# Optimization experiments

Hardware: AMD Instinct MI355X
Metric: run time of the kernel (lower is better)

## Reference

```python
import jax, jax.numpy as jnp
import numpy as np

V, BLOCK, E, H = 50257, 2048, 256, 8
DH = E // H  # head_size = 32
B, T = 2, 2048
SCALE = 1.0 / np.float32(np.sqrt(DH))


def setup_inputs() -> dict:
    key = jax.random.key(0)
    ks = jax.random.split(key, 9)
    s = 0.02
    return {
        "idx": jax.random.randint(ks[0], (B, T), 0, V),
        "targets": jax.random.randint(ks[1], (B, T), 0, V),
        "tok_emb": jax.random.normal(ks[2], (V, E), jnp.float32) * s,
        "pos_emb": jax.random.normal(ks[3], (BLOCK, E), jnp.float32) * s,
        "Wq": jax.random.normal(ks[4], (H, E, DH), jnp.float32) * s,
        "Wk": jax.random.normal(ks[5], (H, E, DH), jnp.float32) * s,
        "Wv": jax.random.normal(ks[6], (H, E, DH), jnp.float32) * s,
        "Wlm": jax.random.normal(ks[7], (V, E), jnp.float32) * s,
        "blm": jnp.zeros((V,), jnp.float32),
    }


def reference(idx, targets, tok_emb, pos_emb, Wq, Wk, Wv, Wlm, blm):
    t = idx.shape[1]
    x = tok_emb[idx] + pos_emb[:t]  # [B,T,E]
    # all heads batched (original loops over heads; same math)
    q = jnp.einsum('bte,hed->bhtd', x, Wq)
    k = jnp.einsum('bte,hed->bhtd', x, Wk)
    v = jnp.einsum('bte,hed->bhtd', x, Wv)
    scores = jnp.einsum('bhqd,bhkd->bhqk', q, k) * SCALE  # [B,H,T,T]
    causal = jnp.tril(jnp.ones((t, t), dtype=bool))
    # faithful to original: tril then masked_fill(scores == 0, -inf)
    scores = jnp.where(causal, scores, 0.0)
    scores = jnp.where(scores == 0.0, -jnp.inf, scores)
    # faithful to original bug: softmax over the QUERY axis (torch dim=1 of [b,t,t])
    attn = jax.nn.softmax(scores, axis=2)
    out = jnp.einsum('bhqk,bhkd->bqhd', attn, v).reshape(idx.shape[0], t, E)  # concat heads
    logits = out @ Wlm.T + blm  # [B,T,V]
    logp = jax.nn.log_softmax(logits, axis=-1)
    loss = -jnp.take_along_axis(logp, targets[..., None], axis=-1).mean()
    return logits, loss
```

## Files before the change

kernel.cpp:

```cpp
#include <hip/hip_runtime.h>
#include <hip/hip_bf16.h>
#include <cstdint>
#include <cstddef>

typedef __bf16 bf16x8 __attribute__((ext_vector_type(8)));
typedef __bf16 bf16x4 __attribute__((ext_vector_type(4)));
typedef float  f32x4  __attribute__((ext_vector_type(4)));
typedef float  f32x16 __attribute__((ext_vector_type(16)));

#define SCALE_QK 0.17677669529663687f
#define V_SIZE 50257
#define T_SEQ  2048
#define E_DIM  256
#define NROWS  4096
#define NNB    393
#define NPAD   (NNB * 128)

__device__ __forceinline__ f32x4 mfma16(bf16x8 a, bf16x8 b, f32x4 c) {
    return __builtin_amdgcn_mfma_f32_16x16x32_bf16(a, b, c, 0, 0, 0);
}
__device__ __forceinline__ f32x16 mfma32(bf16x8 a, bf16x8 b, f32x16 c) {
    return __builtin_amdgcn_mfma_f32_32x32x16_bf16(a, b, c, 0, 0, 0);
}

#define GLOAD_LDS16(gptr, lptr) \
    __builtin_amdgcn_global_load_lds((const __attribute__((address_space(1))) void*)(gptr), \
                                     (__attribute__((address_space(3))) void*)(lptr), 16, 0, 0)

#define ASM_VMCNT0 asm volatile("s_waitcnt vmcnt(0)" ::: "memory")

#define PREP_EMBED 1024
#define PREP_WQKV  (PREP_EMBED + 768)
#define PREP_CVT   (PREP_WQKV + 12576)
#define PREP_ZERO  (PREP_CVT + 128)
__global__ void __launch_bounds__(256)
k_prep(const int* __restrict__ idx, const float* __restrict__ tok,
       const float* __restrict__ pos, __bf16* __restrict__ X,
       const float* __restrict__ Wq, const float* __restrict__ Wk,
       const float* __restrict__ Wv, __bf16* __restrict__ Wo,
       const float* __restrict__ Wlm, __bf16* __restrict__ WlmB,
       float* __restrict__ Dcol) {
    const int bx = blockIdx.x, tid = threadIdx.x;
    if (bx < PREP_EMBED) {
        int row = bx * 4 + (tid >> 6);
        int tl = row & (T_SEQ - 1);
        int tk = idx[row];
        int e = (tid & 63) * 4;
        f32x4 a = *(const f32x4*)(tok + (size_t)tk * E_DIM + e);
        f32x4 p = *(const f32x4*)(pos + (size_t)tl * E_DIM + e);
        bf16x4 o;
#pragma unroll
        for (int i = 0; i < 4; ++i) o[i] = (__bf16)(a[i] + p[i]);
        *(bf16x4*)(X + (size_t)row * E_DIM + e) = o;
    } else if (bx < PREP_WQKV) {
        int n = bx - PREP_EMBED;
        int sel = n >> 8, hd = n & 255, h = hd >> 5, d = hd & 31;
        const float* W = (sel == 0) ? Wq : (sel == 1) ? Wk : Wv;
        Wo[(size_t)n * E_DIM + tid] = (__bf16)W[((size_t)h * E_DIM + tid) * 32 + d];
    } else if (bx < PREP_CVT) {
        size_t i = ((size_t)(bx - PREP_WQKV) * 256 + tid) * 4;
        bf16x4 o = {};
        if (i + 4 <= (size_t)V_SIZE * E_DIM) {
            f32x4 v = *(const f32x4*)(Wlm + i);
#pragma unroll
            for (int j = 0; j < 4; ++j) o[j] = (__bf16)v[j];
        }
        *(bf16x4*)(WlmB + i) = o;
    } else {
        Dcol[(bx - PREP_CVT) * 256 + tid] = 0.f;
    }
}

template <bool BF16_OUT, bool DO_EPI, int REP>
__global__ void __launch_bounds__(256)
k_gemm_bt(const __bf16* __restrict__ A, const __bf16* __restrict__ B,
          void* __restrict__ Cout, const float* __restrict__ bias,
          float* __restrict__ partials, int M, int N, int K) {
    __shared__ __align__(16) char smem[65536];
    __shared__ __align__(16) float bias_lds[128];
    __shared__ float wsum[128][2];

    const int tid = threadIdx.x;
    const int lane = tid & 63, w = tid >> 6;
    const int wr = w >> 1, wc = w & 1;
    const int bm = blockIdx.x, bn = blockIdx.y;
    const int brow = bm * 128, bcol = bn * 128;
    const int gg = lane >> 4, li = lane & 15;
    const int nt = K >> 6;

    if (DO_EPI && tid < 128) bias_lds[tid] = (bcol + tid < N) ? bias[bcol + tid] : 0.f;

    auto stage = [&](int t, int buf) {
        char* Ab = smem + buf * 32768;
        char* Bb = Ab + 16384;
#pragma unroll
        for (int i = 0; i < 4; ++i) {
            int cb = (w * 4 + i) * 64;
            int c = cb + lane;
            int r = c >> 3, kbs = (c & 7) ^ (r & 7);
            GLOAD_LDS16(A + (size_t)(brow + r) * K + t * 64 + kbs * 8, Ab + cb * 16);
            GLOAD_LDS16(B + (size_t)(bcol + r) * K + t * 64 + kbs * 8, Bb + cb * 16);
        }
    };

    for (int rep = 0; rep < REP; ++rep) {
        f32x4 acc[4][4] = {};

        stage(0, 0);
        ASM_VMCNT0;
        __builtin_amdgcn_s_barrier();
        __builtin_amdgcn_sched_barrier(0);

        int cur = 0;
        for (int t = 0; t < nt; ++t) {
            if (t + 1 < nt) stage(t + 1, cur ^ 1);
            const int cbase = cur * 32768;
#pragma unroll
            for (int ks = 0; ks < 2; ++ks) {
                bf16x8 af[4], bfr[4];
#pragma unroll
                for (int mi = 0; mi < 4; ++mi) {
                    int r = wr * 64 + mi * 16 + li;
                    int kbyte = (ks * 64 + gg * 16) ^ ((r & 7) << 4);
                    af[mi] = *(const bf16x8*)(smem + cbase + r * 128 + kbyte);
                }
#pragma unroll
                for (int ni = 0; ni < 4; ++ni) {
                    int r = wc * 64 + ni * 16 + li;
                    int kbyte = (ks * 64 + gg * 16) ^ ((r & 7) << 4);
                    bfr[ni] = *(const bf16x8*)(smem + cbase + 16384 + r * 128 + kbyte);
                }
#pragma unroll
                for (int mi = 0; mi < 4; ++mi)
#pragma unroll
                    for (int ni = 0; ni < 4; ++ni)
                        acc[mi][ni] = mfma16(bfr[ni], af[mi], acc[mi][ni]);
            }
            ASM_VMCNT0;
            __builtin_amdgcn_s_barrier();
            __builtin_amdgcn_sched_barrier(0);
            cur ^= 1;
        }

        const bool full = (bcol + 128 <= N);
        if constexpr (!DO_EPI) {
#pragma unroll
            for (int mi = 0; mi < 4; ++mi) {
                const size_t mrow = (size_t)(brow + wr * 64 + mi * 16 + li) * N;
#pragma unroll
                for (int ni = 0; ni < 4; ++ni) {
                    int nc = wc * 64 + ni * 16 + gg * 4;
                    f32x4 v = acc[mi][ni];
                    bf16x4 o;
#pragma unroll
                    for (int j = 0; j < 4; ++j) o[j] = (__bf16)v[j];
                    *(bf16x4*)((__bf16*)Cout + mrow + bcol + nc) = o;
                }
            }
        } else if (full) {
#pragma unroll
            for (int mi = 0; mi < 4; ++mi) {
                int row = wr * 64 + mi * 16 + li;
                float s = 0.f;
#pragma unroll
                for (int ni = 0; ni < 4; ++ni) {
                    int colb = (wc * 64 + ni * 16 + gg * 4) * 4;
                    f32x4 v = acc[mi][ni];
                    f32x4 bv = *(const f32x4*)((const char*)bias_lds + colb);
#pragma unroll
                    for (int j = 0; j < 4; ++j) { v[j] += bv[j]; s += __expf(v[j]); }
                    *(f32x4*)(smem + row * 512 + (colb ^ ((row & 7) << 4))) = v;
                }
                s += __shfl_xor(s, 16); s += __shfl_xor(s, 32);
                if (gg == 0) wsum[row][wc] = s;
            }
            __syncthreads();
#pragma unroll
            for (int i = 0; i < 16; ++i) {
                int o = i * 4096 + tid * 16;
                int row = o >> 9, cb = o & 511;
                f32x4 v = *(const f32x4*)(smem + row * 512 + (cb ^ ((row & 7) << 4)));
                *(f32x4*)((float*)Cout + (size_t)(brow + row) * N + bcol + (cb >> 2)) = v;
            }
        } else {
#pragma unroll
            for (int mi = 0; mi < 4; ++mi) {
                const size_t mrow = (size_t)(brow + wr * 64 + mi * 16 + li) * N;
                float s = 0.f;
#pragma unroll
                for (int ni = 0; ni < 4; ++ni) {
                    int nc = wc * 64 + ni * 16 + gg * 4;
#pragma unroll
                    for (int j = 0; j < 4; ++j) {
                        int col = bcol + nc + j;
                        if (col < N) {
                            float v = acc[mi][ni][j] + bias_lds[nc + j];
                            s += __expf(v);
                            ((float*)Cout)[mrow + col] = v;
                        }
                    }
                }
                s += __shfl_xor(s, 16); s += __shfl_xor(s, 32);
                if (gg == 0) wsum[wr * 64 + mi * 16 + li][wc] = s;
            }
        }
        if constexpr (DO_EPI) {
            __syncthreads();
            if (tid < 128)
                partials[(size_t)bn * NROWS + (brow + tid)] = wsum[tid][0] + wsum[tid][1];
        }
        if constexpr (REP > 1) __syncthreads();
    }
}

__global__ void __launch_bounds__(256)
k_pass1(const __bf16* __restrict__ QKV, float* __restrict__ Dcol) {
    int p = blockIdx.x;
    int kt = 0;
    while (p >= 16 - kt) { p -= 16 - kt; ++kt; }
    const int qc = kt + p;
    const int bh = blockIdx.y;
    const int b = bh >> 3, h = bh & 7;
    const int tid = threadIdx.x, lane = tid & 63, w = tid >> 6;
    const int g = lane >> 5, li = lane & 31;
    __shared__ __align__(16) __bf16 Klds[4 * 128 * 8];
    __shared__ __align__(16) __bf16 Qlds[4 * 128 * 8];

    const size_t baseQ = ((size_t)b * T_SEQ) * 768 + h * 32;
    const size_t baseK = baseQ + 256;

#pragma unroll
    for (int i = 0; i < 2; ++i) {
        int c = i * 256 + tid; int k = c >> 2, db = c & 3;
        *(bf16x8*)(Klds + (db * 128 + k) * 8) =
            *(const bf16x8*)(QKV + baseK + (size_t)(kt * 128 + k) * 768 + db * 8);
        *(bf16x8*)(Qlds + (db * 128 + k) * 8) =
            *(const bf16x8*)(QKV + baseQ + (size_t)(qc * 128 + k) * 768 + db * 8);
    }
    __syncthreads();

    float csum = 0.f;
    const int kglob = kt * 128 + w * 32 + li;
#pragma unroll
    for (int qs = 0; qs < 4; ++qs) {
        f32x16 sacc = {};
#pragma unroll
        for (int ks = 0; ks < 2; ++ks) {
            bf16x8 aq = *(const bf16x8*)(Qlds + ((ks * 2 + g) * 128 + qs * 32 + li) * 8);
            bf16x8 bk = *(const bf16x8*)(Klds + ((ks * 2 + g) * 128 + w * 32 + li) * 8);
            sacc = mfma32(aq, bk, sacc);
        }
#pragma unroll
        for (int r = 0; r < 16; ++r) {
            int qrow = qc * 128 + qs * 32 + ((r & 3) + 8 * (r >> 2) + 4 * g);
            if (kglob <= qrow) csum += __expf(sacc[r] * SCALE_QK);
        }
    }
    csum += __shfl_xor(csum, 32);
    if (g == 0) atomicAdd(&Dcol[(size_t)bh * T_SEQ + kglob], csum);
}

__global__ void __launch_bounds__(256)
k_pass2(const __bf16* __restrict__ QKV, const float* __restrict__ Dcol,
        float* __restrict__ Yf0, float* __restrict__ Yf1) {
    const int p = blockIdx.x, bh = blockIdx.y;
    const int pi = p >> 1, par = p & 1;
    const int b = bh >> 3, h = bh & 7;
    const int tid = threadIdx.x, lane = tid & 63, w = tid >> 6;
    const int g = lane >> 5, li = lane & 31;
    float* __restrict__ Yf = par ? Yf1 : Yf0;
    __shared__ __align__(16) __bf16 Qlds[4 * 128 * 8];
    __shared__ __align__(16) __bf16 Klds[4 * 128 * 8];
    __shared__ __align__(16) __bf16 UT[16 * 32 * 8];
    __shared__ __align__(16) __bf16 Plds[4][32 * 136];

    const size_t baseQ = ((size_t)b * T_SEQ) * 768 + h * 32;
    const size_t baseK = baseQ + 256;
    const size_t baseV = baseQ + 512;

#pragma unroll
    for (int ti = 0; ti < 2; ++ti) {
        const int qt = ti ? (15 - pi) : pi;
        __syncthreads();
#pragma unroll
        for (int i = 0; i < 2; ++i) {
            int c = i * 256 + tid; int q = c >> 2, db = c & 3;
            *(bf16x8*)(Qlds + (db * 128 + q) * 8) =
                *(const bf16x8*)(QKV + baseQ + (size_t)(qt * 128 + q) * 768 + db * 8);
        }
        f32x16 oacc = {};
        const int qrow = qt * 128 + w * 32 + li;

        for (int kc = par; kc <= qt; kc += 2) {
            __syncthreads();
#pragma unroll
            for (int i = 0; i < 2; ++i) {
                int c = i * 256 + tid; int k = c >> 2, db = c & 3;
                *(bf16x8*)(Klds + (db * 128 + k) * 8) =
                    *(const bf16x8*)(QKV + baseK + (size_t)(kc * 128 + k) * 768 + db * 8);
            }
#pragma unroll
            for (int i = 0; i < 4; ++i) {
                int c = i * 256 + tid; int k = c & 127, d4 = c >> 7;
                float rD = 1.0f / Dcol[(size_t)bh * T_SEQ + kc * 128 + k];
                bf16x4 v4 = *(const bf16x4*)(QKV + baseV + (size_t)(kc * 128 + k) * 768 + d4 * 4);
                int kb = k >> 3, j = k & 7;
#pragma unroll
                for (int t2 = 0; t2 < 4; ++t2)
                    UT[((size_t)kb * 32 + d4 * 4 + t2) * 8 + j] = (__bf16)((float)v4[t2] * rD);
            }
            __syncthreads();

#pragma unroll
            for (int ksub = 0; ksub < 4; ++ksub) {
                int kbase = kc * 128 + ksub * 32;
                f32x16 sacc = {};
#pragma unroll
                for (int ks = 0; ks < 2; ++ks) {
                    bf16x8 ak = *(const bf16x8*)(Klds + ((ks * 2 + g) * 128 + ksub * 32 + li) * 8);
                    bf16x8 bq = *(const bf16x8*)(Qlds + ((ks * 2 + g) * 128 + w * 32 + li) * 8);
                    sacc = mfma32(ak, bq, sacc);
                }
                float pv[16];
#pragma unroll
                for (int r = 0; r < 16; ++r) {
                    int kk = kbase + (r & 3) + 8 * (r >> 2) + 4 * g;
                    pv[r] = (kk <= qrow) ? __expf(sacc[r] * SCALE_QK) : 0.f;
                }
#pragma unroll
                for (int t2 = 0; t2 < 4; ++t2) {
                    bf16x4 pk;
#pragma unroll
                    for (int e = 0; e < 4; ++e) pk[e] = (__bf16)pv[4 * t2 + e];
                    *(bf16x4*)(&Plds[w][li * 136 + ksub * 32 + 8 * t2 + 4 * g]) = pk;
                }
            }
#pragma unroll
            for (int ks16 = 0; ks16 < 8; ++ks16) {
                bf16x8 ap = *(const bf16x8*)(&Plds[w][li * 136 + ks16 * 16 + g * 8]);
                bf16x8 bu = *(const bf16x8*)(UT + ((ks16 * 2 + g) * 32 + li) * 8);
                oacc = mfma32(ap, bu, oacc);
            }
        }
#pragma unroll
        for (int r = 0; r < 16; ++r) {
            int q = qt * 128 + w * 32 + (r & 3) + 8 * (r >> 2) + 4 * g;
            Yf[((size_t)b * T_SEQ + q) * E_DIM + h * 32 + li] = oacc[r];
        }
    }
}

__global__ void k_ycvt(const float* __restrict__ a, const float* __restrict__ b,
                       __bf16* __restrict__ y, int n4) {
    int i = blockIdx.x * 256 + threadIdx.x;
    if (i < n4) {
        f32x4 va = ((const f32x4*)a)[i], vb = ((const f32x4*)b)[i];
        bf16x4 o;
#pragma unroll
        for (int j = 0; j < 4; ++j) o[j] = (__bf16)(va[j] + vb[j]);
        ((bf16x4*)y)[i] = o;
    }
}

__global__ void k_rowlse(const float* __restrict__ partials, const float* __restrict__ logits,
                         const int* __restrict__ tgt, float* __restrict__ rowloss) {
    int r = blockIdx.x * 256 + threadIdx.x;
    float s = 0.f;
    for (int i = 0; i < NNB; ++i) s += partials[(size_t)i * NROWS + r];
    float lse = logf(s);
    rowloss[r] = lse - logits[(size_t)r * V_SIZE + tgt[r]];
}

__global__ void k_loss(const float* __restrict__ rowloss, float* __restrict__ out) {
    __shared__ float red[4];
    float s = 0.f;
    for (int i = threadIdx.x; i < NROWS; i += 256) s += rowloss[i];
    for (int m = 1; m < 64; m <<= 1) s += __shfl_xor(s, m);
    if ((threadIdx.x & 63) == 0) red[threadIdx.x >> 6] = s;
    __syncthreads();
    if (threadIdx.x == 0) out[0] = (red[0] + red[1] + red[2] + red[3]) / (float)NROWS;
}

extern "C" void kernel_launch(void* const* d_in, const int* in_sizes, int n_in,
                              void* d_out, int out_size, void* d_ws, size_t ws_size,
                              hipStream_t stream) {
    const int*   idx = (const int*)d_in[0];
    const int*   tgt = (const int*)d_in[1];
    const float* tok = (const float*)d_in[2];
    const float* pos = (const float*)d_in[3];
    const float* Wq  = (const float*)d_in[4];
    const float* Wk  = (const float*)d_in[5];
    const float* Wv  = (const float*)d_in[6];
    const float* Wlm = (const float*)d_in[7];
    const float* blm = (const float*)d_in[8];

    float* logits = (float*)d_out;
    float* loss   = logits + (size_t)NROWS * V_SIZE;

    char* ws = (char*)d_ws;
    __bf16* X        = (__bf16*)ws; ws += (size_t)NROWS * E_DIM * 2;
    __bf16* Wqkv     = (__bf16*)ws; ws += (size_t)768 * E_DIM * 2;
    __bf16* QKV      = (__bf16*)ws; ws += (size_t)NROWS * 768 * 2;
    float*  Dcol     = (float*)ws;  ws += (size_t)16 * T_SEQ * 4;
    __bf16* Y        = (__bf16*)ws; ws += (size_t)NROWS * E_DIM * 2;
    float*  Yf0      = (float*)ws;  ws += (size_t)NROWS * E_DIM * 4;
    float*  Yf1      = (float*)ws;  ws += (size_t)NROWS * E_DIM * 4;
    __bf16* WlmB     = (__bf16*)ws; ws += (size_t)NPAD * E_DIM * 2;
    float*  partials = (float*)ws;  ws += (size_t)NNB * NROWS * 4;
    float*  rowloss  = (float*)ws;  ws += (size_t)NROWS * 4;

    k_prep<<<PREP_ZERO, 256, 0, stream>>>(idx, tok, pos, X, Wq, Wk, Wv, Wqkv,
                                          Wlm, WlmB, Dcol);
    k_gemm_bt<true, false, 1><<<dim3(NROWS / 128, 768 / 128), 256, 0, stream>>>(
        X, Wqkv, QKV, nullptr, nullptr, NROWS, 768, E_DIM);
    k_pass1<<<dim3(136, 16), 256, 0, stream>>>(QKV, Dcol);
    k_pass2<<<dim3(16, 16), 256, 0, stream>>>(QKV, Dcol, Yf0, Yf1);
    k_ycvt<<<(NROWS * E_DIM / 4 + 255) / 256, 256, 0, stream>>>(Yf0, Yf1, Y, NROWS * E_DIM / 4);
    k_gemm_bt<false, true, 1><<<dim3(NROWS / 128, NNB), 256, 0, stream>>>(
        Y, WlmB, logits, blm, partials, NROWS, V_SIZE, E_DIM);
    k_rowlse<<<NROWS / 256, 256, 0, stream>>>(partials, logits, tgt, rowloss);
    k_loss<<<1, 256, 0, stream>>>(rowloss, loss);
}
```

Before: 482.5 us.

## Single-buffer GEMM with compile-time K, higher occupancy and direct epilogue stores

```diff
diff --git a/kernel.cpp b/kernel.cpp
--- a/kernel.cpp
+++ b/kernel.cpp
@@ -26,8 +26,6 @@
 #define GLOAD_LDS16(gptr, lptr) \
     __builtin_amdgcn_global_load_lds((const __attribute__((address_space(1))) void*)(gptr), \
                                      (__attribute__((address_space(3))) void*)(lptr), 16, 0, 0)
-
-#define ASM_VMCNT0 asm volatile("s_waitcnt vmcnt(0)" ::: "memory")
 
 #define PREP_EMBED 1024
 #define PREP_WQKV  (PREP_EMBED + 768)
@@ -71,12 +69,13 @@
     }
 }
 
-template <bool BF16_OUT, bool DO_EPI, int REP>
-__global__ void __launch_bounds__(256)
+template <bool BF16_OUT, bool DO_EPI, int KK>
+__global__ void __launch_bounds__(256, 4)
 k_gemm_bt(const __bf16* __restrict__ A, const __bf16* __restrict__ B,
           void* __restrict__ Cout, const float* __restrict__ bias,
-          float* __restrict__ partials, int M, int N, int K) {
-    __shared__ __align__(16) char smem[65536];
+          float* __restrict__ partials, int M, int N) {
+    __shared__ __align__(16) __bf16 Alds[128 * 64];
+    __shared__ __align__(16) __bf16 Blds[128 * 64];
     __shared__ __align__(16) float bias_lds[128];
     __shared__ float wsum[128][2];
 
@@ -86,130 +85,104 @@
     const int bm = blockIdx.x, bn = blockIdx.y;
     const int brow = bm * 128, bcol = bn * 128;
     const int gg = lane >> 4, li = lane & 15;
-    const int nt = K >> 6;
+
+    f32x4 acc[4][4] = {};
 
     if (DO_EPI && tid < 128) bias_lds[tid] = (bcol + tid < N) ? bias[bcol + tid] : 0.f;
 
-    auto stage = [&](int t, int buf) {
-        char* Ab = smem + buf * 32768;
-        char* Bb = Ab + 16384;
+#pragma unroll
+    for (int t = 0; t < KK / 64; ++t) {
 #pragma unroll
         for (int i = 0; i < 4; ++i) {
             int cb = (w * 4 + i) * 64;
             int c = cb + lane;
             int r = c >> 3, kbs = (c & 7) ^ (r & 7);
-            GLOAD_LDS16(A + (size_t)(brow + r) * K + t * 64 + kbs * 8, Ab + cb * 16);
-            GLOAD_LDS16(B + (size_t)(bcol + r) * K + t * 64 + kbs * 8, Bb + cb * 16);
-        }
-    };
-
-    for (int rep = 0; rep < REP; ++rep) {
-        f32x4 acc[4][4] = {};
-
-        stage(0, 0);
-        ASM_VMCNT0;
-        __builtin_amdgcn_s_barrier();
-        __builtin_amdgcn_sched_barrier(0);
-
-        int cur = 0;
-        for (int t = 0; t < nt; ++t) {
-            if (t + 1 < nt) stage(t + 1, cur ^ 1);
-            const int cbase = cur * 32768;
-#pragma unroll
-            for (int ks = 0; ks < 2; ++ks) {
-                bf16x8 af[4], bfr[4];
-#pragma unroll
-                for (int mi = 0; mi < 4; ++mi) {
-                    int r = wr * 64 + mi * 16 + li;
-                    int kbyte = (ks * 64 + gg * 16) ^ ((r & 7) << 4);
-                    af[mi] = *(const bf16x8*)(smem + cbase + r * 128 + kbyte);
-                }
-#pragma unroll
-                for (int ni = 0; ni < 4; ++ni) {
-                    int r = wc * 64 + ni * 16 + li;
-                    int kbyte = (ks * 64 + gg * 16) ^ ((r & 7) << 4);
-                    bfr[ni] = *(const bf16x8*)(smem + cbase + 16384 + r * 128 + kbyte);
-                }
-#pragma unroll
-                for (int mi = 0; mi < 4; ++mi)
-#pragma unroll
-                    for (int ni = 0; ni < 4; ++ni)
-                        acc[mi][ni] = mfma16(bfr[ni], af[mi], acc[mi][ni]);
-            }
-            ASM_VMCNT0;
-            __builtin_amdgcn_s_barrier();
-            __builtin_amdgcn_sched_barrier(0);
-            cur ^= 1;
-        }
-
-        const bool full = (bcol + 128 <= N);
-        if constexpr (!DO_EPI) {
+            GLOAD_LDS16(A + (size_t)(brow + r) * KK + t * 64 + kbs * 8, (char*)Alds + cb * 16);
+            GLOAD_LDS16(B + (size_t)(bcol + r) * KK + t * 64 + kbs * 8, (char*)Blds + cb * 16);
+        }
+        __syncthreads();
+#pragma unroll
+        for (int ks = 0; ks < 2; ++ks) {
+            bf16x8 af[4], bfr[4];
 #pragma unroll
             for (int mi = 0; mi < 4; ++mi) {
-                const size_t mrow = (size_t)(brow + wr * 64 + mi * 16 + li) * N;
-#pragma unroll
-                for (int ni = 0; ni < 4; ++ni) {
-                    int nc = wc * 64 + ni * 16 + gg * 4;
-                    f32x4 v = acc[mi][ni];
+                int r = wr * 64 + mi * 16 + li;
+                int kbyte = (ks * 64 + gg * 16) ^ ((r & 7) << 4);
+                af[mi] = *(const bf16x8*)((const char*)Alds + r * 128 + kbyte);
+            }
+#pragma unroll
+            for (int ni = 0; ni < 4; ++ni) {
+                int r = wc * 64 + ni * 16 + li;
+                int kbyte = (ks * 64 + gg * 16) ^ ((r & 7) << 4);
+                bfr[ni] = *(const bf16x8*)((const char*)Blds + r * 128 + kbyte);
+            }
+#pragma unroll
+            for (int mi = 0; mi < 4; ++mi)
+#pragma unroll
+                for (int ni = 0; ni < 4; ++ni)
+                    acc[mi][ni] = mfma16(bfr[ni], af[mi], acc[mi][ni]);
+        }
+        if (t + 1 < KK / 64) __syncthreads();
+    }
+
+    const bool full = (bcol + 128 <= N);
+    if (full) {
+#pragma unroll
+        for (int mi = 0; mi < 4; ++mi) {
+            const size_t mrow = (size_t)(brow + wr * 64 + mi * 16 + li) * N;
+            float s = 0.f;
+#pragma unroll
+            for (int ni = 0; ni < 4; ++ni) {
+                int nc = wc * 64 + ni * 16 + gg * 4;
+                f32x4 v = acc[mi][ni];
+                if constexpr (DO_EPI) {
+                    f32x4 bv = *(const f32x4*)&bias_lds[nc];
+#pragma unroll
+                    for (int j = 0; j < 4; ++j) { v[j] += bv[j]; s += __expf(v[j]); }
+                }
+                if constexpr (BF16_OUT) {
                     bf16x4 o;
 #pragma unroll
                     for (int j = 0; j < 4; ++j) o[j] = (__bf16)v[j];
                     *(bf16x4*)((__bf16*)Cout + mrow + bcol + nc) = o;
-                }
-            }
-        } else if (full) {
-#pragma unroll
-            for (int mi = 0; mi < 4; ++mi) {
-                int row = wr * 64 + mi * 16 + li;
-                float s = 0.f;
-#pragma unroll
-                for (int ni = 0; ni < 4; ++ni) {
-                    int colb = (wc * 64 + ni * 16 + gg * 4) * 4;
-                    f32x4 v = acc[mi][ni];
-                    f32x4 bv = *(const f32x4*)((const char*)bias_lds + colb);
-#pragma unroll
-                    for (int j = 0; j < 4; ++j) { v[j] += bv[j]; s += __expf(v[j]); }
-                    *(f32x4*)(smem + row * 512 + (colb ^ ((row & 7) << 4))) = v;
-                }
-                s += __shfl_xor(s, 16); s += __shfl_xor(s, 32);
-                if (gg == 0) wsum[row][wc] = s;
-            }
-            __syncthreads();
-#pragma unroll
-            for (int i = 0; i < 16; ++i) {
-                int o = i * 4096 + tid * 16;
-                int row = o >> 9, cb = o & 511;
-                f32x4 v = *(const f32x4*)(smem + row * 512 + (cb ^ ((row & 7) << 4)));
-                *(f32x4*)((float*)Cout + (size_t)(brow + row) * N + bcol + (cb >> 2)) = v;
-            }
-        } else {
-#pragma unroll
-            for (int mi = 0; mi < 4; ++mi) {
-                const size_t mrow = (size_t)(brow + wr * 64 + mi * 16 + li) * N;
-                float s = 0.f;
-#pragma unroll
-                for (int ni = 0; ni < 4; ++ni) {
-                    int nc = wc * 64 + ni * 16 + gg * 4;
-#pragma unroll
-                    for (int j = 0; j < 4; ++j) {
-                        int col = bcol + nc + j;
-                        if (col < N) {
-                            float v = acc[mi][ni][j] + bias_lds[nc + j];
-                            s += __expf(v);
-                            ((float*)Cout)[mrow + col] = v;
-                        }
-                    }
-                }
+                } else {
+                    *(f32x4*)((float*)Cout + mrow + bcol + nc) = v;
+                }
+            }
+            if constexpr (DO_EPI) {
                 s += __shfl_xor(s, 16); s += __shfl_xor(s, 32);
                 if (gg == 0) wsum[wr * 64 + mi * 16 + li][wc] = s;
             }
         }
-        if constexpr (DO_EPI) {
-            __syncthreads();
-            if (tid < 128)
-                partials[(size_t)bn * NROWS + (brow + tid)] = wsum[tid][0] + wsum[tid][1];
-        }
-        if constexpr (REP > 1) __syncthreads();
+    } else {
+#pragma unroll
+        for (int mi = 0; mi < 4; ++mi) {
+            const size_t mrow = (size_t)(brow + wr * 64 + mi * 16 + li) * N;
+            float s = 0.f;
+#pragma unroll
+            for (int ni = 0; ni < 4; ++ni) {
+                int nc = wc * 64 + ni * 16 + gg * 4;
+#pragma unroll
+                for (int j = 0; j < 4; ++j) {
+                    int col = bcol + nc + j;
+                    if (col < N) {
+                        float v = acc[mi][ni][j];
+                        if constexpr (DO_EPI) { v += bias_lds[nc + j]; s += __expf(v); }
+                        if constexpr (BF16_OUT) ((__bf16*)Cout)[mrow + col] = (__bf16)v;
+                        else                    ((float*)Cout)[mrow + col] = v;
+                    }
+                }
+            }
+            if constexpr (DO_EPI) {
+                s += __shfl_xor(s, 16); s += __shfl_xor(s, 32);
+                if (gg == 0) wsum[wr * 64 + mi * 16 + li][wc] = s;
+            }
+        }
+    }
+    if constexpr (DO_EPI) {
+        __syncthreads();
+        if (tid < 128)
+            partials[(size_t)bn * NROWS + (brow + tid)] = wsum[tid][0] + wsum[tid][1];
     }
 }
 
@@ -411,13 +384,13 @@
 
     k_prep<<<PREP_ZERO, 256, 0, stream>>>(idx, tok, pos, X, Wq, Wk, Wv, Wqkv,
                                           Wlm, WlmB, Dcol);
-    k_gemm_bt<true, false, 1><<<dim3(NROWS / 128, 768 / 128), 256, 0, stream>>>(
-        X, Wqkv, QKV, nullptr, nullptr, NROWS, 768, E_DIM);
+    k_gemm_bt<true, false, E_DIM><<<dim3(NROWS / 128, 768 / 128), 256, 0, stream>>>(
+        X, Wqkv, QKV, nullptr, nullptr, NROWS, 768);
     k_pass1<<<dim3(136, 16), 256, 0, stream>>>(QKV, Dcol);
     k_pass2<<<dim3(16, 16), 256, 0, stream>>>(QKV, Dcol, Yf0, Yf1);
     k_ycvt<<<(NROWS * E_DIM / 4 + 255) / 256, 256, 0, stream>>>(Yf0, Yf1, Y, NROWS * E_DIM / 4);
-    k_gemm_bt<false, true, 1><<<dim3(NROWS / 128, NNB), 256, 0, stream>>>(
-        Y, WlmB, logits, blm, partials, NROWS, V_SIZE, E_DIM);
+    k_gemm_bt<false, true, E_DIM><<<dim3(NROWS / 128, NNB), 256, 0, stream>>>(
+        Y, WlmB, logits, blm, partials, NROWS, V_SIZE);
     k_rowlse<<<NROWS / 256, 256, 0, stream>>>(partials, logits, tgt, rowloss);
     k_loss<<<1, 256, 0, stream>>>(rowloss, loss);
 }
```

New measurement: 443.3 us. -8.1%, faster.
